# Kernel optimization log

Hardware: AMD Instinct MI355X
Metric: run time of the kernel (lower is better)

The kernel has to match this reference:

```python
import jax, jax.numpy as jnp
import numpy as np

B, S, D, H = 8, 1024, 1024, 16
DH = D // H  # per-head dim = 64
SCALE = float(np.sqrt(DH))  # normalize_coeff = sqrt(dim_h_k)


def _ln(x, g, b, eps=1e-5):
    m = jnp.mean(x, axis=-1, keepdims=True)
    v = jnp.mean(jnp.square(x - m), axis=-1, keepdims=True)
    return (x - m) / jnp.sqrt(v + eps) * g + b


def setup_inputs() -> dict:
    key = jax.random.key(0)
    ks = jax.random.split(key, 12)
    w = lambda k, shape: (jax.random.normal(k, shape, dtype=jnp.float32) * 0.02)
    return {
        "X": jax.random.normal(ks[0], (B, S, D), dtype=jnp.float32),
        # stacked per-head projection weights (torch Linear: y = x @ W.T + b -> store as [H, D, DH])
        "Wq": w(ks[1], (H, D, DH)), "bq": jnp.zeros((H, DH), jnp.float32),
        "Wk": w(ks[2], (H, D, DH)), "bk": jnp.zeros((H, DH), jnp.float32),
        "Wv": w(ks[3], (H, D, DH)), "bv": jnp.zeros((H, DH), jnp.float32),
        "pre_g": jnp.ones((D,), jnp.float32), "pre_b": jnp.zeros((D,), jnp.float32),
        "post_g": jnp.ones((D,), jnp.float32), "post_b": jnp.zeros((D,), jnp.float32),
        "W1": w(ks[4], (D, 2 * D)), "b1": jnp.zeros((2 * D,), jnp.float32),
        "ln1_g": jnp.ones((2 * D,), jnp.float32), "ln1_b": jnp.zeros((2 * D,), jnp.float32),
        "W2": w(ks[5], (2 * D, D)), "b2": jnp.zeros((D,), jnp.float32),
        "ln2_g": jnp.ones((D,), jnp.float32), "ln2_b": jnp.zeros((D,), jnp.float32),
    }


def reference(X, Wq, bq, Wk, bk, Wv, bv, pre_g, pre_b, post_g, post_b,
              W1, b1, ln1_g, ln1_b, W2, b2, ln2_g, ln2_b):
    # pre-LN + multi-head attention (all heads batched instead of python loop)
    t = _ln(X, pre_g, pre_b)
    q = jnp.einsum('bsd,hdk->bhsk', t, Wq) + bq[:, None, :]   # [B,H,S,DH]
    k = jnp.einsum('bsd,hdk->bhsk', t, Wk) + bk[:, None, :]
    v = jnp.einsum('bsd,hdk->bhsk', t, Wv) + bv[:, None, :]
    scores = jnp.einsum('bhqd,bhkd->bhqk', q, k) / SCALE       # [B,H,S,S]
    p = jax.nn.softmax(scores, axis=-1)
    o = jnp.einsum('bhqk,bhkd->bhqd', p, v)                    # [B,H,S,DH]
    o = o.transpose(0, 2, 1, 3).reshape(B, S, D)               # concat heads
    X = X + o
    # post-LN + MLP (Linear -> LN -> GELU -> Linear -> LN -> GELU)
    t2 = _ln(X, post_g, post_b)
    h = jax.nn.gelu(_ln(t2 @ W1 + b1, ln1_g, ln1_b), approximate=False)
    h = jax.nn.gelu(_ln(h @ W2 + b2, ln2_g, ln2_b), approximate=False)
    return X + h
```

## Files before the change

### kernel.cpp

```cpp
#include <hip/hip_runtime.h>

typedef __attribute__((ext_vector_type(8))) short s16x8;
typedef __attribute__((ext_vector_type(8))) unsigned short u16x8;
typedef __attribute__((ext_vector_type(4))) unsigned short u16x4;
typedef __attribute__((ext_vector_type(4))) float f32x4;

__device__ __forceinline__ unsigned short f2bf(float f) {
  union { float f; unsigned int u; } v; v.f = f;
  unsigned int r = (v.u + 0x7FFFu + ((v.u >> 16) & 1u)) >> 16;
  return (unsigned short)r;
}
__device__ __forceinline__ float bf2f(unsigned short h) {
  union { unsigned int u; float f; } v; v.u = ((unsigned int)h) << 16;
  return v.f;
}
__device__ __forceinline__ float gelu(float x) {
  return 0.5f * x * (1.f + erff(x * 0.70710678118654752f));
}
__device__ __forceinline__ float fexp2(float x) {
  float r; asm("v_exp_f32 %0, %1" : "=v"(r) : "v"(x)); return r;
}

__device__ __forceinline__ void gld16(const void* g, void* l) {
  __builtin_amdgcn_global_load_lds(
      (const __attribute__((address_space(1))) unsigned int*)g,
      (__attribute__((address_space(3))) unsigned int*)l, 16, 0, 0);
}

__device__ __forceinline__ float blk_sum(float v, float* red, int tid, int nw) {
#pragma unroll
  for (int m = 32; m >= 1; m >>= 1) v += __shfl_xor(v, m);
  __syncthreads();
  if ((tid & 63) == 0) red[tid >> 6] = v;
  __syncthreads();
  float t = 0.f;
  for (int i = 0; i < nw; ++i) t += red[i];
  return t;
}

__global__ __launch_bounds__(256) void k_tr(
    const float* __restrict__ in, unsigned short* __restrict__ out,
    int inRS, int outRS, long inBS, long outBS) {
  __shared__ float t[32][33];
  const float* ip = in + (size_t)blockIdx.z * inBS;
  unsigned short* op = out + (size_t)blockIdx.z * outBS;
  const int r0 = blockIdx.y * 32, c0 = blockIdx.x * 32;
  const int tid = threadIdx.x;
  const int r = tid >> 3, c4 = (tid & 7) * 4;
  const f32x4 v = *(const f32x4*)(ip + (size_t)(r0 + r) * inRS + c0 + c4);
#pragma unroll
  for (int i = 0; i < 4; ++i) t[r][c4 + i] = v[i];
  __syncthreads();
  u16x4 o;
#pragma unroll
  for (int i = 0; i < 4; ++i) o[i] = f2bf(t[c4 + i][r]);
  *(u16x4*)(op + (size_t)(c0 + r) * outRS + r0 + c4) = o;
}

__global__ __launch_bounds__(256) void k_bias3(
    const float* __restrict__ a, const float* __restrict__ b,
    const float* __restrict__ c, float* __restrict__ o) {
  int i = blockIdx.x * 256 + threadIdx.x;
  if (i >= 3072) return;
  o[i] = (i < 1024) ? a[i] : ((i < 2048) ? b[i - 1024] : c[i - 2048]);
}

__global__ __launch_bounds__(256) void k_pre_ln(
    const float* __restrict__ X, const float* __restrict__ g,
    const float* __restrict__ bta, unsigned short* __restrict__ out) {
  __shared__ float red[4];
  const int row = blockIdx.x, tid = threadIdx.x;
  const f32x4 x = *(const f32x4*)(X + (size_t)row * 1024 + tid * 4);
  float s = x[0] + x[1] + x[2] + x[3];
  s = blk_sum(s, red, tid, 4);
  const float mean = s * (1.f / 1024.f);
  f32x4 d;
#pragma unroll
  for (int i = 0; i < 4; ++i) d[i] = x[i] - mean;
  float sq = d[0] * d[0] + d[1] * d[1] + d[2] * d[2] + d[3] * d[3];
  sq = blk_sum(sq, red, tid, 4);
  const float rstd = rsqrtf(sq * (1.f / 1024.f) + 1e-5f);
  const f32x4 gv = *(const f32x4*)(g + tid * 4);
  const f32x4 bv = *(const f32x4*)(bta + tid * 4);
  u16x4 o;
#pragma unroll
  for (int i = 0; i < 4; ++i) o[i] = f2bf(d[i] * rstd * gv[i] + bv[i]);
  *(u16x4*)(out + (size_t)row * 1024 + tid * 4) = o;
}

__global__ __launch_bounds__(256) void k_res_ln(
    const float* __restrict__ X, const unsigned short* __restrict__ attn,
    const float* __restrict__ g, const float* __restrict__ bta,
    float* __restrict__ X1, unsigned short* __restrict__ t2) {
  __shared__ float red[4];
  const int row = blockIdx.x, tid = threadIdx.x;
  const f32x4 x = *(const f32x4*)(X + (size_t)row * 1024 + tid * 4);
  const u16x4 a = *(const u16x4*)(attn + (size_t)row * 1024 + tid * 4);
  f32x4 x1;
#pragma unroll
  for (int i = 0; i < 4; ++i) x1[i] = x[i] + bf2f(a[i]);
  *(f32x4*)(X1 + (size_t)row * 1024 + tid * 4) = x1;
  float s = x1[0] + x1[1] + x1[2] + x1[3];
  s = blk_sum(s, red, tid, 4);
  const float mean = s * (1.f / 1024.f);
  f32x4 d;
#pragma unroll
  for (int i = 0; i < 4; ++i) d[i] = x1[i] - mean;
  float sq = d[0] * d[0] + d[1] * d[1] + d[2] * d[2] + d[3] * d[3];
  sq = blk_sum(sq, red, tid, 4);
  const float rstd = rsqrtf(sq * (1.f / 1024.f) + 1e-5f);
  const f32x4 gv = *(const f32x4*)(g + tid * 4);
  const f32x4 bv = *(const f32x4*)(bta + tid * 4);
  u16x4 o;
#pragma unroll
  for (int i = 0; i < 4; ++i) o[i] = f2bf(d[i] * rstd * gv[i] + bv[i]);
  *(u16x4*)(t2 + (size_t)row * 1024 + tid * 4) = o;
}

__global__ __launch_bounds__(256) void k_ln_gelu(
    const unsigned short* __restrict__ in, const float* __restrict__ g,
    const float* __restrict__ bta, unsigned short* __restrict__ out) {
  __shared__ float red[4];
  const int row = blockIdx.x, tid = threadIdx.x;
  const u16x8 iv = *(const u16x8*)(in + (size_t)row * 2048 + tid * 8);
  float v[8];
  float s = 0.f;
#pragma unroll
  for (int i = 0; i < 8; ++i) { v[i] = bf2f(iv[i]); s += v[i]; }
  s = blk_sum(s, red, tid, 4);
  const float mean = s * (1.f / 2048.f);
  float sq = 0.f;
#pragma unroll
  for (int i = 0; i < 8; ++i) { v[i] -= mean; sq += v[i] * v[i]; }
  sq = blk_sum(sq, red, tid, 4);
  const float rstd = rsqrtf(sq * (1.f / 2048.f) + 1e-5f);
  u16x8 o;
#pragma unroll
  for (int i = 0; i < 8; ++i) {
    float t = v[i] * rstd * g[tid * 8 + i] + bta[tid * 8 + i];
    o[i] = f2bf(gelu(t));
  }
  *(u16x8*)(out + (size_t)row * 2048 + tid * 8) = o;
}

__global__ __launch_bounds__(256) void k_final(
    const unsigned short* __restrict__ in, const float* __restrict__ g,
    const float* __restrict__ bta, float* __restrict__ io) {
  __shared__ float red[4];
  const int row = blockIdx.x, tid = threadIdx.x;
  const u16x4 iv = *(const u16x4*)(in + (size_t)row * 1024 + tid * 4);
  float v[4];
  float s = 0.f;
#pragma unroll
  for (int i = 0; i < 4; ++i) { v[i] = bf2f(iv[i]); s += v[i]; }
  s = blk_sum(s, red, tid, 4);
  const float mean = s * (1.f / 1024.f);
  float sq = 0.f;
#pragma unroll
  for (int i = 0; i < 4; ++i) { v[i] -= mean; sq += v[i] * v[i]; }
  sq = blk_sum(sq, red, tid, 4);
  const float rstd = rsqrtf(sq * (1.f / 1024.f) + 1e-5f);
  const f32x4 gv = *(const f32x4*)(g + tid * 4);
  const f32x4 bv = *(const f32x4*)(bta + tid * 4);
  f32x4 xi = *(const f32x4*)(io + (size_t)row * 1024 + tid * 4);
#pragma unroll
  for (int i = 0; i < 4; ++i)
    xi[i] += gelu(v[i] * rstd * gv[i] + bv[i]);
  *(f32x4*)(io + (size_t)row * 1024 + tid * 4) = xi;
}

__global__ __launch_bounds__(512) void k_gemm2(
    const unsigned short* __restrict__ A, const unsigned short* __restrict__ Bt,
    const float* __restrict__ bias, unsigned short* __restrict__ C,
    int M, int N, int K, int vsplit, unsigned short* __restrict__ VtO) {
  extern __shared__ __align__(16) unsigned short lds[];
  const int tid = threadIdx.x;
  const int w = tid >> 6, l = tid & 63;
  const int wm = w >> 1, wn = w & 1;
  const int gx = gridDim.x;
  int flat = blockIdx.y * gx + blockIdx.x;
  const int nwg = gx * gridDim.y;
  if ((nwg & 7) == 0) flat = (flat & 7) * (nwg >> 3) + (flat >> 3);
  const int m0 = (flat / gx) * 256, n0 = (flat % gx) * 128;

  const f32x4 z4 = {0.f, 0.f, 0.f, 0.f};
  f32x4 acc[4][4];
#pragma unroll
  for (int i = 0; i < 4; ++i)
#pragma unroll
    for (int j = 0; j < 4; ++j) acc[i][j] = z4;

#define STAGE_G2(t, d)                                                              \
  {                                                                                 \
    const int kb = (t) * 64;                                                        \
    _Pragma("unroll") for (int i = 0; i < 4; ++i) {                                 \
      const int s = i * 512 + tid;                                                  \
      const int row = s >> 3, cs = s & 7;                                           \
      gld16(A + (size_t)(m0 + row) * K + kb + ((cs ^ (row & 7)) << 3),              \
            lds + (d) * 24576 + s * 8);                                             \
    }                                                                               \
    _Pragma("unroll") for (int i = 0; i < 2; ++i) {                                 \
      const int s = i * 512 + tid;                                                  \
      const int row = s >> 3, cs = s & 7;                                           \
      gld16(Bt + (size_t)(n0 + row) * K + kb + ((cs ^ (row & 7)) << 3),             \
            lds + (d) * 24576 + 16384 + s * 8);                                     \
    }                                                                               \
  }

  const int nt = K >> 6;
  STAGE_G2(0, 0);
  STAGE_G2(1, 1);

  for (int t = 0; t < nt; ++t) {
    const int d = t % 3;
    if (t + 2 < nt) {
      const int d2 = (t + 2) % 3;
      STAGE_G2(t + 2, d2);
      asm volatile("s_waitcnt vmcnt(12)" ::: "memory");
    } else if (t + 1 < nt) {
      asm volatile("s_waitcnt vmcnt(6)" ::: "memory");
    } else {
      asm volatile("s_waitcnt vmcnt(0)" ::: "memory");
    }
    __syncthreads();

    const unsigned short* Ab = lds + d * 24576;
    const unsigned short* Bb = Ab + 16384;
    __builtin_amdgcn_s_setprio(1);
#pragma unroll
    for (int ks = 0; ks < 2; ++ks) {
      const int cs = ks * 4 + (l >> 4);
      s16x8 a[4], b[4];
#pragma unroll
      for (int m = 0; m < 4; ++m) {
        const int row = wm * 64 + m * 16 + (l & 15);
        a[m] = *(const s16x8*)(Ab + row * 64 + ((cs ^ (row & 7)) << 3));
      }
#pragma unroll
      for (int n = 0; n < 4; ++n) {
        const int row = wn * 64 + n * 16 + (l & 15);
        b[n] = *(const s16x8*)(Bb + row * 64 + ((cs ^ (row & 7)) << 3));
      }
#pragma unroll
      for (int m = 0; m < 4; ++m)
#pragma unroll
        for (int n = 0; n < 4; ++n)
          acc[m][n] = __builtin_amdgcn_mfma_f32_16x16x32_bf16(a[m], b[n], acc[m][n], 0, 0, 0);
    }
    __builtin_amdgcn_s_setprio(0);
    __syncthreads();
  }
#undef STAGE_G2

  const int rbase = m0 + wm * 64 + ((l >> 4) << 2);
  const int cbase = n0 + wn * 64 + (l & 15);
#pragma unroll
  for (int n = 0; n < 4; ++n) {
    const int c = cbase + n * 16;
    const float bb = bias[c];
    if ((n0 + wn * 64 + n * 16) < vsplit) {
#pragma unroll
      for (int m = 0; m < 4; ++m)
#pragma unroll
        for (int r = 0; r < 4; ++r)
          C[(size_t)(rbase + m * 16 + r) * N + c] = f2bf(acc[m][n][r] + bb);
    } else {
      const int cc = c - vsplit;
      const int hh = cc >> 6, dd = cc & 63;
#pragma unroll
      for (int m = 0; m < 4; ++m) {
        const int rr = rbase + m * 16;
        u16x4 o;
#pragma unroll
        for (int r = 0; r < 4; ++r) o[r] = f2bf(acc[m][n][r] + bb);
        *(u16x4*)(VtO + ((size_t)((rr >> 10) * 16 + hh)) * 65536 + dd * 1024 + (rr & 1023)) = o;
      }
    }
  }
}

__device__ __forceinline__ int swz(int r, int c) {
  return r * 64 + (c ^ ((r & 7) << 3));
}

__global__ __launch_bounds__(256) void k_attn3(
    const unsigned short* __restrict__ qkv, const unsigned short* __restrict__ Vt,
    unsigned short* __restrict__ O) {
  int bid = blockIdx.x;
  bid = (bid & 7) * 256 + (bid >> 3);
  const int qt = bid & 15, h = (bid >> 4) & 15, b = bid >> 8;
  const int tid = threadIdx.x, w = tid >> 6, l = tid & 63;
  const int arow = l & 15, kcol = (l >> 4) * 8;

  __shared__ __align__(16) unsigned short Kb[2][64 * 64];
  __shared__ __align__(16) unsigned short Vb[2][64 * 64];
  __shared__ __align__(16) unsigned short Ps[4][16 * 64];
  unsigned short* ps = &Ps[w][0];

  const unsigned short* qb = qkv + (size_t)b * 1024 * 3072 + h * 64;
  const unsigned short* kb = qb + 1024;
  const unsigned short* vt = Vt + ((size_t)(b * 16 + h)) * 65536;
  const int q0 = qt * 64 + w * 16;

  const float c2 = 0.125f * 1.44269504088896f;

  s16x8 qa[2];
#pragma unroll
  for (int kh = 0; kh < 2; ++kh) {
    s16x8 q = *(const s16x8*)(qb + (size_t)(q0 + arow) * 3072 + kh * 32 + kcol);
#pragma unroll
    for (int j = 0; j < 8; ++j)
      q[j] = (short)f2bf(bf2f((unsigned short)q[j]) * c2);
    qa[kh] = q;
  }
  s16x8 ones;
#pragma unroll
  for (int j = 0; j < 8; ++j) ones[j] = (short)0x3F80;

  const int srow = tid >> 3;
  const int sce = 8 * ((tid & 7) ^ (srow & 7));
  const int sdst = srow * 64 + (tid & 7) * 8;

#pragma unroll
  for (int i = 0; i < 2; ++i) {
    gld16(kb + (size_t)(i * 32 + srow) * 3072 + sce, Kb[0] + i * 2048 + sdst);
    gld16(vt + (size_t)(i * 32 + srow) * 1024 + sce, Vb[0] + i * 2048 + sdst);
  }
  __syncthreads();

  const f32x4 z4 = {0.f, 0.f, 0.f, 0.f};
  f32x4 oacc[4];
#pragma unroll
  for (int i = 0; i < 4; ++i) oacc[i] = z4;
  f32x4 lacc = z4;
  float mrun[4];
#pragma unroll
  for (int r = 0; r < 4; ++r) mrun[r] = -1e30f;

  for (int kc = 0; kc < 16; ++kc) {
    const int cur = kc & 1;
    if (kc < 15) {
      const int key1 = (kc + 1) * 64;
#pragma unroll
      for (int i = 0; i < 2; ++i) {
        gld16(kb + (size_t)(key1 + i * 32 + srow) * 3072 + sce, Kb[cur ^ 1] + i * 2048 + sdst);
        gld16(vt + (size_t)(i * 32 + srow) * 1024 + key1 + sce, Vb[cur ^ 1] + i * 2048 + sdst);
      }
    }
    f32x4 sacc[4];
#pragma unroll
    for (int t = 0; t < 4; ++t) {
      s16x8 k0 = *(const s16x8*)(Kb[cur] + swz(t * 16 + arow, kcol));
      s16x8 k1 = *(const s16x8*)(Kb[cur] + swz(t * 16 + arow, 32 + kcol));
      f32x4 s = z4;
      s = __builtin_amdgcn_mfma_f32_16x16x32_bf16(qa[0], k0, s, 0, 0, 0);
      s = __builtin_amdgcn_mfma_f32_16x16x32_bf16(qa[1], k1, s, 0, 0, 0);
      sacc[t] = s;
    }
    float rmax[4];
#pragma unroll
    for (int r = 0; r < 4; ++r) {
      float m = fmaxf(fmaxf(sacc[0][r], sacc[1][r]), fmaxf(sacc[2][r], sacc[3][r]));
#pragma unroll
      for (int msk = 8; msk >= 1; msk >>= 1) m = fmaxf(m, __shfl_xor(m, msk));
      rmax[r] = m;
    }
    const float need = fmaxf(fmaxf(rmax[0] - mrun[0], rmax[1] - mrun[1]),
                             fmaxf(rmax[2] - mrun[2], rmax[3] - mrun[3]));
    if (!__all(need <= 8.f)) {
      float sc[4];
#pragma unroll
      for (int r = 0; r < 4; ++r) {
        const float nm = fmaxf(mrun[r], rmax[r]);
        sc[r] = fexp2(mrun[r] - nm);
        mrun[r] = nm;
      }
#pragma unroll
      for (int r = 0; r < 4; ++r) {
        lacc[r] *= sc[r];
#pragma unroll
        for (int dg = 0; dg < 4; ++dg) oacc[dg][r] *= sc[r];
      }
    }
#pragma unroll
    for (int t = 0; t < 4; ++t)
#pragma unroll
      for (int r = 0; r < 4; ++r) {
        const float p = fexp2(sacc[t][r] - mrun[r]);
        ps[swz(((l >> 4) << 2) + r, t * 16 + arow)] = f2bf(p);
      }
    s16x8 pa[2];
#pragma unroll
    for (int kh = 0; kh < 2; ++kh)
      pa[kh] = *(const s16x8*)(ps + swz(arow, kh * 32 + kcol));
    lacc = __builtin_amdgcn_mfma_f32_16x16x32_bf16(pa[0], ones, lacc, 0, 0, 0);
    lacc = __builtin_amdgcn_mfma_f32_16x16x32_bf16(pa[1], ones, lacc, 0, 0, 0);
#pragma unroll
    for (int dg = 0; dg < 4; ++dg) {
      s16x8 v0 = *(const s16x8*)(Vb[cur] + swz(dg * 16 + arow, kcol));
      s16x8 v1 = *(const s16x8*)(Vb[cur] + swz(dg * 16 + arow, 32 + kcol));
      oacc[dg] = __builtin_amdgcn_mfma_f32_16x16x32_bf16(pa[0], v0, oacc[dg], 0, 0, 0);
      oacc[dg] = __builtin_amdgcn_mfma_f32_16x16x32_bf16(pa[1], v1, oacc[dg], 0, 0, 0);
    }
    __syncthreads();
  }

  float inv[4];
#pragma unroll
  for (int r = 0; r < 4; ++r) inv[r] = 1.f / lacc[r];
#pragma unroll
  for (int dg = 0; dg < 4; ++dg)
#pragma unroll
    for (int r = 0; r < 4; ++r) {
      const int row = q0 + ((l >> 4) << 2) + r;
      O[(size_t)(b * 1024 + row) * 1024 + h * 64 + dg * 16 + arow] = f2bf(oacc[dg][r] * inv[r]);
    }
}

extern "C" void kernel_launch(void* const* d_in, const int* in_sizes, int n_in,
                              void* d_out, int out_size, void* d_ws, size_t ws_size,
                              hipStream_t stream) {
  const float* X = (const float*)d_in[0];
  const float* Wq = (const float*)d_in[1];
  const float* bq = (const float*)d_in[2];
  const float* Wk = (const float*)d_in[3];
  const float* bk = (const float*)d_in[4];
  const float* Wv = (const float*)d_in[5];
  const float* bv = (const float*)d_in[6];
  const float* pre_g = (const float*)d_in[7];
  const float* pre_b = (const float*)d_in[8];
  const float* post_g = (const float*)d_in[9];
  const float* post_b = (const float*)d_in[10];
  const float* W1 = (const float*)d_in[11];
  const float* b1 = (const float*)d_in[12];
  const float* ln1_g = (const float*)d_in[13];
  const float* ln1_b = (const float*)d_in[14];
  const float* W2 = (const float*)d_in[15];
  const float* b2 = (const float*)d_in[16];
  const float* ln2_g = (const float*)d_in[17];
  const float* ln2_b = (const float*)d_in[18];
  float* out = (float*)d_out;

  char* ws = (char*)d_ws;
  const size_t MB = (size_t)1 << 20;
  unsigned short* t_bf = (unsigned short*)(ws);
  unsigned short* attn_o = (unsigned short*)(ws);
  unsigned short* mlp2 = (unsigned short*)(ws);
  unsigned short* qkv = (unsigned short*)(ws + 16 * MB);
  unsigned short* mlp1 = (unsigned short*)(ws + 16 * MB);
  unsigned short* Vt = (unsigned short*)(ws + 64 * MB);
  unsigned short* h1 = (unsigned short*)(ws + 48 * MB);
  unsigned short* t2 = (unsigned short*)(ws + 80 * MB);
  unsigned short* Wqkvt = (unsigned short*)(ws + 96 * MB);
  unsigned short* W1t = (unsigned short*)(ws + 102 * MB);
  unsigned short* W2t = (unsigned short*)(ws + 106 * MB);
  float* biasq = (float*)(ws + 110 * MB);

  hipFuncSetAttribute((const void*)k_gemm2,
                      hipFuncAttributeMaxDynamicSharedMemorySize, 3 * 49152);

  k_tr<<<dim3(2, 32, 16), 256, 0, stream>>>(Wq, Wqkvt, 64, 1024, 65536, 65536);
  k_tr<<<dim3(2, 32, 16), 256, 0, stream>>>(Wk, Wqkvt + 1048576, 64, 1024, 65536, 65536);
  k_tr<<<dim3(2, 32, 16), 256, 0, stream>>>(Wv, Wqkvt + 2097152, 64, 1024, 65536, 65536);
  k_tr<<<dim3(64, 32, 1), 256, 0, stream>>>(W1, W1t, 2048, 1024, 0, 0);
  k_tr<<<dim3(32, 64, 1), 256, 0, stream>>>(W2, W2t, 1024, 2048, 0, 0);
  k_bias3<<<12, 256, 0, stream>>>(bq, bk, bv, biasq);

  k_pre_ln<<<8192, 256, 0, stream>>>(X, pre_g, pre_b, t_bf);
  k_gemm2<<<dim3(24, 32), 512, 3 * 49152, stream>>>(t_bf, Wqkvt, biasq, qkv, 8192, 3072, 1024, 2048, Vt);
  k_attn3<<<2048, 256, 0, stream>>>(qkv, Vt, attn_o);
  k_res_ln<<<8192, 256, 0, stream>>>(X, attn_o, post_g, post_b, out, t2);
  k_gemm2<<<dim3(16, 32), 512, 3 * 49152, stream>>>(t2, W1t, b1, mlp1, 8192, 2048, 1024, 1 << 30, nullptr);
  k_ln_gelu<<<8192, 256, 0, stream>>>(mlp1, ln1_g, ln1_b, h1);
  k_gemm2<<<dim3(8, 32), 512, 3 * 49152, stream>>>(h1, W2t, b2, mlp2, 8192, 1024, 2048, 1 << 30, nullptr);
  k_final<<<8192, 256, 0, stream>>>(mlp2, ln2_g, ln2_b, out);
}
```

Measured before the change: 519.1 us.

## Shrink GEMM tile to 128x128 with 256 threads and double-buffered static LDS

The GEMM kernel changes from 256x128 tiles with 8 waves and a 3-stage dynamic-LDS pipeline to 128x128 tiles with 4 waves and a 2-stage static LDS buffer (64 KB per block). Each block now uses less LDS, so more blocks can be resident per CU and the grid has twice as many workgroups. The loop uses raw s_barrier with explicit waitcnt instead of __syncthreads. In exchange, each block loads more operand data per FLOP and has a shallower prefetch depth. The XCD remap is now applied unconditionally.

```diff
diff --git a/kernel.cpp b/kernel.cpp
--- a/kernel.cpp
+++ b/kernel.cpp
@@ -169,19 +169,19 @@
   *(f32x4*)(io + (size_t)row * 1024 + tid * 4) = xi;
 }
 
-__global__ __launch_bounds__(512) void k_gemm2(
+__global__ __launch_bounds__(256) void k_gemm3(
     const unsigned short* __restrict__ A, const unsigned short* __restrict__ Bt,
     const float* __restrict__ bias, unsigned short* __restrict__ C,
     int M, int N, int K, int vsplit, unsigned short* __restrict__ VtO) {
-  extern __shared__ __align__(16) unsigned short lds[];
+  __shared__ __align__(16) unsigned short lds[2][16384];
   const int tid = threadIdx.x;
   const int w = tid >> 6, l = tid & 63;
   const int wm = w >> 1, wn = w & 1;
   const int gx = gridDim.x;
   int flat = blockIdx.y * gx + blockIdx.x;
   const int nwg = gx * gridDim.y;
-  if ((nwg & 7) == 0) flat = (flat & 7) * (nwg >> 3) + (flat >> 3);
-  const int m0 = (flat / gx) * 256, n0 = (flat % gx) * 128;
+  flat = (flat & 7) * (nwg >> 3) + (flat >> 3);
+  const int m0 = (flat / gx) * 128, n0 = (flat % gx) * 128;
 
   const f32x4 z4 = {0.f, 0.f, 0.f, 0.f};
   f32x4 acc[4][4];
@@ -190,56 +190,49 @@
 #pragma unroll
     for (int j = 0; j < 4; ++j) acc[i][j] = z4;
 
-#define STAGE_G2(t, d)                                                              \
+#define STG(t, d)                                                                   \
   {                                                                                 \
     const int kb = (t) * 64;                                                        \
     _Pragma("unroll") for (int i = 0; i < 4; ++i) {                                 \
-      const int s = i * 512 + tid;                                                  \
+      const int s = i * 256 + tid;                                                  \
       const int row = s >> 3, cs = s & 7;                                           \
       gld16(A + (size_t)(m0 + row) * K + kb + ((cs ^ (row & 7)) << 3),              \
-            lds + (d) * 24576 + s * 8);                                             \
+            &lds[d][s * 8]);                                                        \
     }                                                                               \
-    _Pragma("unroll") for (int i = 0; i < 2; ++i) {                                 \
-      const int s = i * 512 + tid;                                                  \
+    _Pragma("unroll") for (int i = 0; i < 4; ++i) {                                 \
+      const int s = i * 256 + tid;                                                  \
       const int row = s >> 3, cs = s & 7;                                           \
       gld16(Bt + (size_t)(n0 + row) * K + kb + ((cs ^ (row & 7)) << 3),             \
-            lds + (d) * 24576 + 16384 + s * 8);                                     \
+            &lds[d][8192 + s * 8]);                                                 \
     }                                                                               \
   }
 
   const int nt = K >> 6;
-  STAGE_G2(0, 0);
-  STAGE_G2(1, 1);
-
+  STG(0, 0);
   for (int t = 0; t < nt; ++t) {
-    const int d = t % 3;
-    if (t + 2 < nt) {
-      const int d2 = (t + 2) % 3;
-      STAGE_G2(t + 2, d2);
-      asm volatile("s_waitcnt vmcnt(12)" ::: "memory");
-    } else if (t + 1 < nt) {
-      asm volatile("s_waitcnt vmcnt(6)" ::: "memory");
+    const int cur = t & 1;
+    if (t + 1 < nt) {
+      STG(t + 1, cur ^ 1);
+      asm volatile("s_waitcnt vmcnt(8)" ::: "memory");
     } else {
       asm volatile("s_waitcnt vmcnt(0)" ::: "memory");
     }
-    __syncthreads();
-
-    const unsigned short* Ab = lds + d * 24576;
-    const unsigned short* Bb = Ab + 16384;
+    __builtin_amdgcn_s_barrier();
+    asm volatile("" ::: "memory");
     __builtin_amdgcn_s_setprio(1);
 #pragma unroll
     for (int ks = 0; ks < 2; ++ks) {
-      const int cs = ks * 4 + (l >> 4);
+      const int g = ks * 4 + (l >> 4);
       s16x8 a[4], b[4];
 #pragma unroll
       for (int m = 0; m < 4; ++m) {
         const int row = wm * 64 + m * 16 + (l & 15);
-        a[m] = *(const s16x8*)(Ab + row * 64 + ((cs ^ (row & 7)) << 3));
+        a[m] = *(const s16x8*)&lds[cur][row * 64 + ((g ^ (row & 7)) << 3)];
       }
 #pragma unroll
       for (int n = 0; n < 4; ++n) {
         const int row = wn * 64 + n * 16 + (l & 15);
-        b[n] = *(const s16x8*)(Bb + row * 64 + ((cs ^ (row & 7)) << 3));
+        b[n] = *(const s16x8*)&lds[cur][8192 + row * 64 + ((g ^ (row & 7)) << 3)];
       }
 #pragma unroll
       for (int m = 0; m < 4; ++m)
@@ -248,9 +241,11 @@
           acc[m][n] = __builtin_amdgcn_mfma_f32_16x16x32_bf16(a[m], b[n], acc[m][n], 0, 0, 0);
     }
     __builtin_amdgcn_s_setprio(0);
-    __syncthreads();
-  }
-#undef STAGE_G2
+    asm volatile("s_waitcnt lgkmcnt(0)" ::: "memory");
+    __builtin_amdgcn_s_barrier();
+    asm volatile("" ::: "memory");
+  }
+#undef STG
 
   const int rbase = m0 + wm * 64 + ((l >> 4) << 2);
   const int cbase = n0 + wn * 64 + (l & 15);
@@ -456,9 +451,6 @@
   unsigned short* W2t = (unsigned short*)(ws + 106 * MB);
   float* biasq = (float*)(ws + 110 * MB);
 
-  hipFuncSetAttribute((const void*)k_gemm2,
-                      hipFuncAttributeMaxDynamicSharedMemorySize, 3 * 49152);
-
   k_tr<<<dim3(2, 32, 16), 256, 0, stream>>>(Wq, Wqkvt, 64, 1024, 65536, 65536);
   k_tr<<<dim3(2, 32, 16), 256, 0, stream>>>(Wk, Wqkvt + 1048576, 64, 1024, 65536, 65536);
   k_tr<<<dim3(2, 32, 16), 256, 0, stream>>>(Wv, Wqkvt + 2097152, 64, 1024, 65536, 65536);
@@ -467,11 +459,11 @@
   k_bias3<<<12, 256, 0, stream>>>(bq, bk, bv, biasq);
 
   k_pre_ln<<<8192, 256, 0, stream>>>(X, pre_g, pre_b, t_bf);
-  k_gemm2<<<dim3(24, 32), 512, 3 * 49152, stream>>>(t_bf, Wqkvt, biasq, qkv, 8192, 3072, 1024, 2048, Vt);
+  k_gemm3<<<dim3(24, 64), 256, 0, stream>>>(t_bf, Wqkvt, biasq, qkv, 8192, 3072, 1024, 2048, Vt);
   k_attn3<<<2048, 256, 0, stream>>>(qkv, Vt, attn_o);
   k_res_ln<<<8192, 256, 0, stream>>>(X, attn_o, post_g, post_b, out, t2);
-  k_gemm2<<<dim3(16, 32), 512, 3 * 49152, stream>>>(t2, W1t, b1, mlp1, 8192, 2048, 1024, 1 << 30, nullptr);
+  k_gemm3<<<dim3(16, 64), 256, 0, stream>>>(t2, W1t, b1, mlp1, 8192, 2048, 1024, 1 << 30, nullptr);
   k_ln_gelu<<<8192, 256, 0, stream>>>(mlp1, ln1_g, ln1_b, h1);
-  k_gemm2<<<dim3(8, 32), 512, 3 * 49152, stream>>>(h1, W2t, b2, mlp2, 8192, 1024, 2048, 1 << 30, nullptr);
+  k_gemm3<<<dim3(8, 64), 256, 0, stream>>>(h1, W2t, b2, mlp2, 8192, 1024, 2048, 1 << 30, nullptr);
   k_final<<<8192, 256, 0, stream>>>(mlp2, ln2_g, ln2_b, out);
 }
```

Result: faster. 468.3 us (-9.8%).
